# Performance work log

Hardware: AMD Instinct MI355X
Metric: run time of the kernel (lower is better)

## Reference

```python
import jax, jax.numpy as jnp
import numpy as np

L = 0.24          # lambda step size
K = 0.03          # exp(log 0.03), conductance scale used by forward
NITER = 500       # ctor Niter
DEPS = 0.1


def _g(x, k):
    # Perona-Malik conductance: 1 / (1 + |x^2| / k^2); x real so |x*x| == x*x
    return 1.0 / (1.0 + (x * x) / (k * k))


def setup_inputs() -> dict:
    key = jax.random.key(0)
    k1, k2 = jax.random.split(key)
    guide = jax.random.normal(k1, (2, 3, 512, 512), dtype=jnp.float32)
    initial = jax.random.uniform(k2, (2, 1, 512, 512), dtype=jnp.float32)
    return {"guide": guide, "initial": initial}


def reference(guide, initial):
    # shift branch (jit-safe): forward adds deps if initial.min() <= deps, subtracts at end
    shift = jnp.where(jnp.min(initial) <= DEPS, DEPS, 0.0).astype(initial.dtype)
    depth0 = initial + shift

    # conductance coefficients from guide (mean abs channel gradient), shapes:
    # cv: [B,1,H-1,W], ch: [B,1,H,W-1]
    cv = _g(jnp.mean(jnp.abs(guide[:, :, 1:, :] - guide[:, :, :-1, :]), axis=1, keepdims=True), K)
    ch = _g(jnp.mean(jnp.abs(guide[:, :, :, 1:] - guide[:, :, :, :-1]), axis=1, keepdims=True), K)

    def step(I, _):
        # both diffs computed from the same I (matches torch: dv, dh read before writes;
        # the in-place +/- updates commute, so functional adds give identical math)
        dv = I[:, :, 1:, :] - I[:, :, :-1, :]
        dh = I[:, :, :, 1:] - I[:, :, :, :-1]
        tv = L * cv * dv
        th = L * ch * dh
        I = I.at[:, :, 1:, :].add(-tv)
        I = I.at[:, :, :-1, :].add(tv)
        I = I.at[:, :, :, 1:].add(-th)
        I = I.at[:, :, :, :-1].add(th)
        return I, None

    depth, _ = jax.lax.scan(step, depth0, None, length=NITER)
    y_pred = depth - shift
    return (y_pred, cv, ch)
```

## Files before the change

kernel.cpp:

```cpp
#include <hip/hip_runtime.h>


#define HH 512
#define WW 512
#define NB 2
static constexpr float LAM   = 0.24f;
static constexpr float KCOND = 0.03f;
static constexpr float DEPS_ = 0.1f;
static constexpr int IMG      = HH * WW;
static constexpr int N_DEPTH  = NB * IMG;
static constexpr int CV_PER_B = (HH - 1) * WW;
static constexpr int CH_PER_B = HH * (WW - 1);
static constexpr int N_CV     = NB * CV_PER_B;
static constexpr int N_CH     = NB * CH_PER_B;

static constexpr int T_FUSE = 10, NSS = 50;
static constexpr int TILE_W = 64, TILE_H = 32;
static constexpr int HALO_X = 12, HALO_Y = 10;
static constexpr int RW = TILE_W + 2 * HALO_X;
static constexpr int RH = TILE_H + 2 * HALO_Y;
static constexpr int NQ_ROW = RW / 4;
static constexpr int NQUAD  = NQ_ROW * RH;
static constexpr int SSZ    = (RH + 2) * RW;

static constexpr int NT  = 512;
static constexpr int QPT = 3;
static constexpr int CVW = RW;
static constexpr int CV_SZ = (RH + 1) * CVW;
static constexpr int CHW = RW + 8;
static constexpr int CH_SZ = RH * CHW;
static constexpr int BLOB_BLK = CV_SZ + CH_SZ;

static constexpr int QPT_F = 5;

__device__ __forceinline__ unsigned fkey(float f) {
    unsigned u = __float_as_uint(f);
    return (u & 0x80000000u) ? ~u : (u | 0x80000000u);
}
__device__ __forceinline__ float kinv(unsigned k) {
    return __uint_as_float((k & 0x80000000u) ? (k & 0x7fffffffu) : ~k);
}

__global__ void init_key_kernel(unsigned* key) { *key = 0xFFFFFFFFu; }

__global__ void min_kernel(const float* __restrict__ x, unsigned* key) {
    float m = 3.4e38f;
    for (int idx = blockIdx.x * blockDim.x + threadIdx.x; idx < N_DEPTH;
         idx += gridDim.x * blockDim.x)
        m = fminf(m, x[idx]);
    for (int off = 32; off > 0; off >>= 1) m = fminf(m, __shfl_down(m, off, 64));
    __shared__ float sm[4];
    int lane = threadIdx.x & 63, wv = threadIdx.x >> 6;
    if (lane == 0) sm[wv] = m;
    __syncthreads();
    if (threadIdx.x == 0) {
        float mm = fminf(fminf(sm[0], sm[1]), fminf(sm[2], sm[3]));
        atomicMin(key, fkey(mm));
    }
}

__global__ void coeff_kernel(const float* __restrict__ g, float* __restrict__ cv,
                             float* __restrict__ chh) {
    int idx = blockIdx.x * blockDim.x + threadIdx.x;
    constexpr float kk = KCOND * KCOND;
    if (idx < N_CV) {
        int b = idx / CV_PER_B;
        int r = idx - b * CV_PER_B;
        int i = r >> 9, j = r & (WW - 1);
        const float* gb = g + b * 3 * IMG + i * WW + j;
        float s = 0.f;
#pragma unroll
        for (int c = 0; c < 3; ++c) s += fabsf(gb[c * IMG + WW] - gb[c * IMG]);
        float m = s / 3.0f;
        cv[idx] = 1.0f / (1.0f + (m * m) / kk);
    } else if (idx < N_CV + N_CH) {
        int t = idx - N_CV;
        int b = t / CH_PER_B;
        int r = t - b * CH_PER_B;
        int i = r / (WW - 1);
        int j = r - i * (WW - 1);
        const float* gb = g + b * 3 * IMG + i * WW + j;
        float s = 0.f;
#pragma unroll
        for (int c = 0; c < 3; ++c) s += fabsf(gb[c * IMG + 1] - gb[c * IMG]);
        float m = s / 3.0f;
        chh[t] = 1.0f / (1.0f + (m * m) / kk);
    }
}

__global__ __launch_bounds__(256) void prep_planes(const float* __restrict__ cv_g,
                                                   const float* __restrict__ ch_g,
                                                   float* __restrict__ blob) {
    const int blk = blockIdx.x;
    const int b   = blk >> 7, t = blk & 127;
    const int y0  = (t >> 3) * TILE_H;
    const int x0  = (t & 7) * TILE_W;
    const float* cvb = cv_g + b * CV_PER_B;
    const float* chb = ch_g + b * CH_PER_B;
    float* pv = blob + blk * BLOB_BLK;
    float* ph = pv + CV_SZ;
    for (int i = threadIdx.x; i < CV_SZ; i += 256) {
        int rr = i / CVW, x = i - rr * CVW;
        int gy = y0 - HALO_Y + rr, gx = x0 - HALO_X + x;
        bool ok = (rr >= 1) && (rr <= RH - 1) && (gy >= 1) && (gy <= HH - 1) &&
                  (gx >= 0) && (gx < WW);
        pv[i] = ok ? LAM * cvb[(gy - 1) * WW + gx] : 0.f;
    }
    for (int i = threadIdx.x; i < CH_SZ; i += 256) {
        int rr = i / CHW, xe = i - rr * CHW;
        int gy = y0 - HALO_Y + rr, gxe = x0 - HALO_X + xe;
        bool ok = (xe >= 1) && (xe <= RW - 1) && (gy >= 0) && (gy < HH) &&
                  (gxe >= 1) && (gxe < WW);
        ph[i] = ok ? LAM * chb[gy * (WW - 1) + (gxe - 1)] : 0.f;
    }
}

template <bool ADD_SHIFT, bool SUB_SHIFT>
__global__ __launch_bounds__(NT, 1) void step_fast(
    const float* __restrict__ src, float* __restrict__ dst,
    const float* __restrict__ blob, const unsigned* __restrict__ key) {
    __shared__ float sb[2][SSZ];
    const int blk = blockIdx.x;
    const int b   = blk >> 7, t = blk & 127;
    const int y0  = (t >> 3) * TILE_H;
    const int x0  = (t & 7) * TILE_W;
    const float* srcb = src + b * IMG;
    const float* pv   = blob + blk * BLOB_BLK;
    const float* ph   = pv + CV_SZ;

    float shift = 0.f;
    if (ADD_SHIFT || SUB_SHIFT) shift = (kinv(*key) <= DEPS_) ? DEPS_ : 0.f;
    const int tid = threadIdx.x;

    float v[QPT][4], cu[QPT][4], cd[QPT][4], chq[QPT][5];
    int   roff[QPT], goff[QPT];
    bool  is_int[QPT], in_img[QPT];

#pragma unroll
    for (int q = 0; q < QPT; ++q) {
        int qi   = tid + q * NT;
        bool act = qi < NQUAD;
        int qc   = act ? qi : 0;
        int r    = qc / NQ_ROW;
        int x    = (qc - r * NQ_ROW) * 4;
        roff[q]  = (r + 1) * RW + x;
        int gy = y0 - HALO_Y + r, gx = x0 - HALO_X + x;
        bool gy_in = (gy >= 0) && (gy < HH);
        in_img[q]  = act && gy_in && (gx >= 0) && (gx <= WW - 4);
        goff[q]    = in_img[q] ? (gy * WW + gx) : 0;
        is_int[q]  = act && (r >= HALO_Y) && (r < HALO_Y + TILE_H) &&
                     (x >= HALO_X) && (x < HALO_X + TILE_W);
        float4 a  = *reinterpret_cast<const float4*>(&pv[r * CVW + x]);
        float4 d  = *reinterpret_cast<const float4*>(&pv[(r + 1) * CVW + x]);
        float4 h  = *reinterpret_cast<const float4*>(&ph[r * CHW + x]);
        float  h4 = ph[r * CHW + x + 4];
        float am = act ? 1.f : 0.f;
        cu[q][0] = a.x * am; cu[q][1] = a.y * am; cu[q][2] = a.z * am; cu[q][3] = a.w * am;
        cd[q][0] = d.x * am; cd[q][1] = d.y * am; cd[q][2] = d.z * am; cd[q][3] = d.w * am;
        chq[q][0] = h.x * am; chq[q][1] = h.y * am; chq[q][2] = h.z * am;
        chq[q][3] = h.w * am; chq[q][4] = h4 * am;
        float4 tv = {0.f, 0.f, 0.f, 0.f};
        if (in_img[q]) tv = *reinterpret_cast<const float4*>(srcb + goff[q]);
        if (ADD_SHIFT && in_img[q]) {
            tv.x += shift; tv.y += shift; tv.z += shift; tv.w += shift;
        }
        v[q][0] = tv.x; v[q][1] = tv.y; v[q][2] = tv.z; v[q][3] = tv.w;
    }

    for (int i = tid; i < RW; i += NT) {
        sb[0][i] = 0.f; sb[0][(RH + 1) * RW + i] = 0.f;
        sb[1][i] = 0.f; sb[1][(RH + 1) * RW + i] = 0.f;
    }
#pragma unroll
    for (int q = 0; q < QPT; ++q)
        *reinterpret_cast<float4*>(&sb[0][roff[q]]) =
            float4{v[q][0], v[q][1], v[q][2], v[q][3]};
    __syncthreads();

    int cur = 0;
    for (int it = 0; it < T_FUSE; ++it) {
        float nv[QPT][4];
#pragma unroll
        for (int q = 0; q < QPT; ++q) {
            const float* s = sb[cur];
            float4 up = *reinterpret_cast<const float4*>(&s[roff[q] - RW]);
            float4 dn = *reinterpret_cast<const float4*>(&s[roff[q] + RW]);
            float  lf = s[roff[q] - 1];
            float  rt = s[roff[q] + 4];
            float c0 = v[q][0], c1 = v[q][1], c2 = v[q][2], c3 = v[q][3];
            nv[q][0] = c0 - cu[q][0] * (c0 - up.x) + cd[q][0] * (dn.x - c0)
                          - chq[q][0] * (c0 - lf) + chq[q][1] * (c1 - c0);
            nv[q][1] = c1 - cu[q][1] * (c1 - up.y) + cd[q][1] * (dn.y - c1)
                          - chq[q][1] * (c1 - c0) + chq[q][2] * (c2 - c1);
            nv[q][2] = c2 - cu[q][2] * (c2 - up.z) + cd[q][2] * (dn.z - c2)
                          - chq[q][2] * (c2 - c1) + chq[q][3] * (c3 - c2);
            nv[q][3] = c3 - cu[q][3] * (c3 - up.w) + cd[q][3] * (dn.w - c3)
                          - chq[q][3] * (c3 - c2) + chq[q][4] * (rt - c3);
        }
        int nxt = cur ^ 1;
#pragma unroll
        for (int q = 0; q < QPT; ++q) {
            *reinterpret_cast<float4*>(&sb[nxt][roff[q]]) =
                float4{nv[q][0], nv[q][1], nv[q][2], nv[q][3]};
            v[q][0] = nv[q][0]; v[q][1] = nv[q][1];
            v[q][2] = nv[q][2]; v[q][3] = nv[q][3];
        }
        cur = nxt;
        __syncthreads();
    }

    float* dstb = dst + b * IMG;
#pragma unroll
    for (int q = 0; q < QPT; ++q) {
        if (is_int[q]) {
            float4 o{v[q][0], v[q][1], v[q][2], v[q][3]};
            if (SUB_SHIFT) { o.x -= shift; o.y -= shift; o.z -= shift; o.w -= shift; }
            *reinterpret_cast<float4*>(dstb + goff[q]) = o;
        }
    }
}

template <bool ADD_SHIFT, bool SUB_SHIFT>
__global__ __launch_bounds__(256, 1) void step_fused(
    const float* __restrict__ src, float* __restrict__ dst,
    const float* __restrict__ cv_g, const float* __restrict__ ch_g,
    const unsigned* __restrict__ key) {
    __shared__ float sb[2][SSZ];
    const int blk = blockIdx.x;
    const int b = blk >> 7, t = blk & 127;
    const int y0 = (t >> 3) * TILE_H, x0 = (t & 7) * TILE_W;
    const float* cvb = cv_g + b * CV_PER_B;
    const float* chb = ch_g + b * CH_PER_B;
    const float* srcb = src + b * IMG;
    float* dstb = dst + b * IMG;
    float shift = 0.f;
    if (ADD_SHIFT || SUB_SHIFT) shift = (kinv(*key) <= DEPS_) ? DEPS_ : 0.f;
    const int tid = threadIdx.x;
    float v[QPT_F][4], cu[QPT_F][4], cd[QPT_F][4], chq[QPT_F][5];
    int roff[QPT_F], rr[QPT_F], xx[QPT_F];
    bool act[QPT_F];
#pragma unroll
    for (int q = 0; q < QPT_F; ++q) {
        int qi = tid + q * 256;
        act[q] = qi < NQUAD;
        int qc = act[q] ? qi : 0;
        int r = qc / NQ_ROW;
        int x = (qc - r * NQ_ROW) * 4;
        rr[q] = r; xx[q] = x;
        roff[q] = (r + 1) * RW + x;
        int gy = y0 - HALO_Y + r, gx = x0 - HALO_X + x;
        bool gy_in = (gy >= 0) && (gy < HH);
#pragma unroll
        for (int j = 0; j < 4; ++j) {
            int gxx = gx + j;
            bool gx_in = (gxx >= 0) && (gxx < WW);
            bool vin = act[q] && gy_in && gx_in;
            float val = vin ? srcb[gy * WW + gxx] : 0.f;
            if (ADD_SHIFT) val += shift;
            v[q][j] = vin ? val : 0.f;
            bool up_ok = act[q] && (r >= 1) && (gy >= 1) && (gy < HH) && gx_in;
            cu[q][j] = up_ok ? LAM * cvb[(gy - 1) * WW + gxx] : 0.f;
            bool dn_ok = act[q] && (r <= RH - 2) && (gy >= 0) && (gy < HH - 1) && gx_in;
            cd[q][j] = dn_ok ? LAM * cvb[gy * WW + gxx] : 0.f;
        }
#pragma unroll
        for (int jj = 0; jj < 5; ++jj) {
            int xe = x + jj, gxe = gx + jj;
            bool ok = act[q] && (xe >= 1) && (xe <= RW - 1) && gy_in &&
                      (gxe >= 1) && (gxe < WW);
            chq[q][jj] = ok ? LAM * chb[gy * (WW - 1) + (gxe - 1)] : 0.f;
        }
    }
    for (int i = tid; i < RW; i += 256) {
        sb[0][i] = 0.f; sb[0][(RH + 1) * RW + i] = 0.f;
        sb[1][i] = 0.f; sb[1][(RH + 1) * RW + i] = 0.f;
    }
#pragma unroll
    for (int q = 0; q < QPT_F; ++q)
        if (act[q])
            *reinterpret_cast<float4*>(&sb[0][roff[q]]) =
                float4{v[q][0], v[q][1], v[q][2], v[q][3]};
    __syncthreads();
    int cur = 0;
    for (int it = 0; it < T_FUSE; ++it) {
        float nv[QPT_F][4];
#pragma unroll
        for (int q = 0; q < QPT_F; ++q) {
            const float* s = sb[cur];
            float4 up = *reinterpret_cast<const float4*>(&s[roff[q] - RW]);
            float4 dn = *reinterpret_cast<const float4*>(&s[roff[q] + RW]);
            float lf = s[roff[q] - 1];
            float rt = s[roff[q] + 4];
            float c0 = v[q][0], c1 = v[q][1], c2 = v[q][2], c3 = v[q][3];
            nv[q][0] = c0 - cu[q][0] * (c0 - up.x) + cd[q][0] * (dn.x - c0)
                          - chq[q][0] * (c0 - lf) + chq[q][1] * (c1 - c0);
            nv[q][1] = c1 - cu[q][1] * (c1 - up.y) + cd[q][1] * (dn.y - c1)
                          - chq[q][1] * (c1 - c0) + chq[q][2] * (c2 - c1);
            nv[q][2] = c2 - cu[q][2] * (c2 - up.z) + cd[q][2] * (dn.z - c2)
                          - chq[q][2] * (c2 - c1) + chq[q][3] * (c3 - c2);
            nv[q][3] = c3 - cu[q][3] * (c3 - up.w) + cd[q][3] * (dn.w - c3)
                          - chq[q][3] * (c3 - c2) + chq[q][4] * (rt - c3);
        }
        int nxt = cur ^ 1;
#pragma unroll
        for (int q = 0; q < QPT_F; ++q) {
            if (act[q])
                *reinterpret_cast<float4*>(&sb[nxt][roff[q]]) =
                    float4{nv[q][0], nv[q][1], nv[q][2], nv[q][3]};
            v[q][0] = nv[q][0]; v[q][1] = nv[q][1];
            v[q][2] = nv[q][2]; v[q][3] = nv[q][3];
        }
        cur = nxt;
        __syncthreads();
    }
#pragma unroll
    for (int q = 0; q < QPT_F; ++q) {
        if (!act[q]) continue;
        int r = rr[q], x = xx[q];
        if (r >= HALO_Y && r < HALO_Y + TILE_H && x >= HALO_X && x < HALO_X + TILE_W) {
            int gy = y0 - HALO_Y + r, gx = x0 - HALO_X + x;
            float4 o{v[q][0], v[q][1], v[q][2], v[q][3]};
            if (SUB_SHIFT) { o.x -= shift; o.y -= shift; o.z -= shift; o.w -= shift; }
            *reinterpret_cast<float4*>(dstb + gy * WW + gx) = o;
        }
    }
}

extern "C" void kernel_launch(void* const* d_in, const int* in_sizes, int n_in,
                              void* d_out, int out_size, void* d_ws, size_t ws_size,
                              hipStream_t stream) {
    const float* guide   = (const float*)d_in[0];
    const float* initial = (const float*)d_in[1];
    float* out    = (float*)d_out;
    float* out_y  = out;
    float* out_cv = out + N_DEPTH;
    float* out_ch = out + N_DEPTH + N_CV;

    unsigned* key = (unsigned*)d_ws;
    float* wsf    = (float*)d_ws;
    float* bufA   = wsf + 64;
    float* bufB   = bufA + N_DEPTH;
    float* blob   = bufB + N_DEPTH;

    const size_t need = (size_t)(64 + 2 * N_DEPTH + 256 * BLOB_BLK) * 4;
    const bool fast = ws_size >= need;

    hipLaunchKernelGGL(init_key_kernel, dim3(1), dim3(1), 0, stream, key);
    hipLaunchKernelGGL(min_kernel, dim3(256), dim3(256), 0, stream, initial, key);

    int nco = N_CV + N_CH;
    hipLaunchKernelGGL(coeff_kernel, dim3((nco + 255) / 256), dim3(256), 0, stream,
                       guide, out_cv, out_ch);
    if (fast)
        hipLaunchKernelGGL(prep_planes, dim3(256), dim3(256), 0, stream,
                           out_cv, out_ch, blob);

    float* bufs[2] = {bufA, bufB};
    for (int k = 0; k < NSS; ++k) {
        const float* src = (k == 0) ? initial : bufs[(k + 1) & 1];
        float*       dst = (k == NSS - 1) ? out_y : bufs[k & 1];
        if (fast) {
            if (k == 0)
                hipLaunchKernelGGL((step_fast<true, false>), dim3(256), dim3(NT), 0,
                                   stream, src, dst, blob, key);
            else if (k == NSS - 1)
                hipLaunchKernelGGL((step_fast<false, true>), dim3(256), dim3(NT), 0,
                                   stream, src, dst, blob, key);
            else
                hipLaunchKernelGGL((step_fast<false, false>), dim3(256), dim3(NT), 0,
                                   stream, src, dst, blob, key);
        } else {
            if (k == 0)
                hipLaunchKernelGGL((step_fused<true, false>), dim3(256), dim3(256), 0,
                                   stream, src, dst, out_cv, out_ch, key);
            else if (k == NSS - 1)
                hipLaunchKernelGGL((step_fused<false, true>), dim3(256), dim3(256), 0,
                                   stream, src, dst, out_cv, out_ch, key);
            else
                hipLaunchKernelGGL((step_fused<false, false>), dim3(256), dim3(256), 0,
                                   stream, src, dst, out_cv, out_ch, key);
        }
    }
}
```

Measured before the change: 520.1 us.

## Register-block 4x4 pixels per thread and exchange only tile borders via LDS

Replaces the 1x4 quad-per-thread stencil with 4x4 register blocks per thread. Each thread keeps its interior neighbours in registers and publishes only its top and bottom rows and left and right columns to compact shared-memory edge buffers. Coefficients are precombined into a centre weight, so each update is a 5-term FMA sum. This cuts LDS traffic per iteration and drops block size to 320 threads, at the cost of more registers per thread and a more complex edge-buffer layout.

After: 552.3 us. 6.2% more time.

```diff
diff --git a/kernel.cpp b/kernel.cpp
--- a/kernel.cpp
+++ b/kernel.cpp
@@ -23,13 +23,21 @@
 static constexpr int NQUAD  = NQ_ROW * RH;
 static constexpr int SSZ    = (RH + 2) * RW;
 
-static constexpr int NT  = 512;
-static constexpr int QPT = 3;
 static constexpr int CVW = RW;
 static constexpr int CV_SZ = (RH + 1) * CVW;
 static constexpr int CHW = RW + 8;
 static constexpr int CH_SZ = RH * CHW;
 static constexpr int BLOB_BLK = CV_SZ + CH_SZ;
+
+static constexpr int NBAND = RH / 4;
+static constexpr int NUNIT = NBAND * NQ_ROW;
+static constexpr int NT2   = 320;
+static constexpr int RROW  = 92;
+static constexpr int RT_O  = 0;
+static constexpr int RBS_O = RT_O + (NBAND + 1) * RROW;
+static constexpr int CL_O  = RBS_O + (NBAND + 1) * RROW;
+static constexpr int CRS_O = CL_O + NBAND * 23 * 4;
+static constexpr int BUF_SZ = CRS_O + NBAND * 23 * 4;
 
 static constexpr int QPT_F = 5;
 
@@ -116,106 +124,149 @@
 }
 
 template <bool ADD_SHIFT, bool SUB_SHIFT>
-__global__ __launch_bounds__(NT, 1) void step_fast(
+__global__ __launch_bounds__(NT2, 1) void step_reg(
     const float* __restrict__ src, float* __restrict__ dst,
     const float* __restrict__ blob, const unsigned* __restrict__ key) {
-    __shared__ float sb[2][SSZ];
-    const int blk = blockIdx.x;
-    const int b   = blk >> 7, t = blk & 127;
-    const int y0  = (t >> 3) * TILE_H;
-    const int x0  = (t & 7) * TILE_W;
-    const float* srcb = src + b * IMG;
-    const float* pv   = blob + blk * BLOB_BLK;
-    const float* ph   = pv + CV_SZ;
+    __shared__ float sb[2 * BUF_SZ];
+    const int blk   = blockIdx.x;
+    const int b_img = blk >> 7, t = blk & 127;
+    const int y0 = (t >> 3) * TILE_H, x0 = (t & 7) * TILE_W;
+    const float* srcb = src + b_img * IMG;
+    const float* pv = blob + blk * BLOB_BLK;
+    const float* ph = pv + CV_SZ;
 
     float shift = 0.f;
     if (ADD_SHIFT || SUB_SHIFT) shift = (kinv(*key) <= DEPS_) ? DEPS_ : 0.f;
-    const int tid = threadIdx.x;
-
-    float v[QPT][4], cu[QPT][4], cd[QPT][4], chq[QPT][5];
-    int   roff[QPT], goff[QPT];
-    bool  is_int[QPT], in_img[QPT];
-
-#pragma unroll
-    for (int q = 0; q < QPT; ++q) {
-        int qi   = tid + q * NT;
-        bool act = qi < NQUAD;
-        int qc   = act ? qi : 0;
-        int r    = qc / NQ_ROW;
-        int x    = (qc - r * NQ_ROW) * 4;
-        roff[q]  = (r + 1) * RW + x;
-        int gy = y0 - HALO_Y + r, gx = x0 - HALO_X + x;
-        bool gy_in = (gy >= 0) && (gy < HH);
-        in_img[q]  = act && gy_in && (gx >= 0) && (gx <= WW - 4);
-        goff[q]    = in_img[q] ? (gy * WW + gx) : 0;
-        is_int[q]  = act && (r >= HALO_Y) && (r < HALO_Y + TILE_H) &&
-                     (x >= HALO_X) && (x < HALO_X + TILE_W);
-        float4 a  = *reinterpret_cast<const float4*>(&pv[r * CVW + x]);
-        float4 d  = *reinterpret_cast<const float4*>(&pv[(r + 1) * CVW + x]);
-        float4 h  = *reinterpret_cast<const float4*>(&ph[r * CHW + x]);
-        float  h4 = ph[r * CHW + x + 4];
-        float am = act ? 1.f : 0.f;
-        cu[q][0] = a.x * am; cu[q][1] = a.y * am; cu[q][2] = a.z * am; cu[q][3] = a.w * am;
-        cd[q][0] = d.x * am; cd[q][1] = d.y * am; cd[q][2] = d.z * am; cd[q][3] = d.w * am;
-        chq[q][0] = h.x * am; chq[q][1] = h.y * am; chq[q][2] = h.z * am;
-        chq[q][3] = h.w * am; chq[q][4] = h4 * am;
-        float4 tv = {0.f, 0.f, 0.f, 0.f};
-        if (in_img[q]) tv = *reinterpret_cast<const float4*>(srcb + goff[q]);
-        if (ADD_SHIFT && in_img[q]) {
-            tv.x += shift; tv.y += shift; tv.z += shift; tv.w += shift;
-        }
-        v[q][0] = tv.x; v[q][1] = tv.y; v[q][2] = tv.z; v[q][3] = tv.w;
-    }
-
-    for (int i = tid; i < RW; i += NT) {
-        sb[0][i] = 0.f; sb[0][(RH + 1) * RW + i] = 0.f;
-        sb[1][i] = 0.f; sb[1][(RH + 1) * RW + i] = 0.f;
-    }
-#pragma unroll
-    for (int q = 0; q < QPT; ++q)
-        *reinterpret_cast<float4*>(&sb[0][roff[q]]) =
-            float4{v[q][0], v[q][1], v[q][2], v[q][3]};
+
+    const int  tid = threadIdx.x;
+    const bool act = tid < NUNIT;
+    const int  u  = act ? tid : 0;
+    const int  bb = u / NQ_ROW;
+    const int  qc = u - bb * NQ_ROW;
+    const int  x  = qc * 4;
+
+    float v[4][4], vert[5][4], hz[4][5], cc[4][4];
+    int   goffr[4];
+    bool  rin[4];
+
+    const int up_o = RBS_O + bb * RROW + x;
+    const int dn_o = RT_O + (bb + 1) * RROW + x;
+    const int lf_o = CRS_O + (bb * 23 + qc) * 4;
+    const int rt_o = CL_O + (bb * 23 + qc + 1) * 4;
+    const int wt_o = RT_O + bb * RROW + x;
+    const int wb_o = RBS_O + (bb + 1) * RROW + x;
+    const int wl_o = CL_O + (bb * 23 + qc) * 4;
+    const int wr_o = CRS_O + (bb * 23 + qc + 1) * 4;
+
+    if (act) {
+#pragma unroll
+        for (int k = 0; k < 5; ++k) {
+            float4 a = *reinterpret_cast<const float4*>(&pv[(4 * bb + k) * CVW + x]);
+            vert[k][0] = a.x; vert[k][1] = a.y; vert[k][2] = a.z; vert[k][3] = a.w;
+        }
+#pragma unroll
+        for (int k = 0; k < 4; ++k) {
+            int r = 4 * bb + k;
+            float4 h = *reinterpret_cast<const float4*>(&ph[r * CHW + x]);
+            hz[k][0] = h.x; hz[k][1] = h.y; hz[k][2] = h.z; hz[k][3] = h.w;
+            hz[k][4] = ph[r * CHW + x + 4];
+        }
+#pragma unroll
+        for (int k = 0; k < 4; ++k)
+#pragma unroll
+            for (int j = 0; j < 4; ++j)
+                cc[k][j] = 1.f - (vert[k][j] + vert[k + 1][j] + hz[k][j] + hz[k][j + 1]);
+
+        int  gx    = x0 - HALO_X + x;
+        bool gx_in = (gx >= 0) && (gx <= WW - 4);
+#pragma unroll
+        for (int k = 0; k < 4; ++k) {
+            int r  = 4 * bb + k;
+            int gy = y0 - HALO_Y + r;
+            rin[k]   = gx_in && (gy >= 0) && (gy < HH);
+            goffr[k] = rin[k] ? (gy * WW + gx) : 0;
+            float4 tv = {0.f, 0.f, 0.f, 0.f};
+            if (rin[k]) tv = *reinterpret_cast<const float4*>(srcb + goffr[k]);
+            if (ADD_SHIFT && rin[k]) {
+                tv.x += shift; tv.y += shift; tv.z += shift; tv.w += shift;
+            }
+            v[k][0] = tv.x; v[k][1] = tv.y; v[k][2] = tv.z; v[k][3] = tv.w;
+        }
+    }
+
+    for (int i = tid; i < RROW; i += NT2) {
+        sb[RT_O + NBAND * RROW + i] = 0.f;
+        sb[RBS_O + i] = 0.f;
+        sb[BUF_SZ + RT_O + NBAND * RROW + i] = 0.f;
+        sb[BUF_SZ + RBS_O + i] = 0.f;
+    }
+    for (int i = tid; i < NBAND; i += NT2) {
+#pragma unroll
+        for (int j = 0; j < 4; ++j) {
+            sb[CL_O + (i * 23 + 22) * 4 + j] = 0.f;
+            sb[CRS_O + (i * 23) * 4 + j] = 0.f;
+            sb[BUF_SZ + CL_O + (i * 23 + 22) * 4 + j] = 0.f;
+            sb[BUF_SZ + CRS_O + (i * 23) * 4 + j] = 0.f;
+        }
+    }
+    if (act) {
+        *reinterpret_cast<float4*>(&sb[wt_o]) = float4{v[0][0], v[0][1], v[0][2], v[0][3]};
+        *reinterpret_cast<float4*>(&sb[wb_o]) = float4{v[3][0], v[3][1], v[3][2], v[3][3]};
+        *reinterpret_cast<float4*>(&sb[wl_o]) = float4{v[0][0], v[1][0], v[2][0], v[3][0]};
+        *reinterpret_cast<float4*>(&sb[wr_o]) = float4{v[0][3], v[1][3], v[2][3], v[3][3]};
+    }
     __syncthreads();
 
     int cur = 0;
     for (int it = 0; it < T_FUSE; ++it) {
-        float nv[QPT][4];
-#pragma unroll
-        for (int q = 0; q < QPT; ++q) {
-            const float* s = sb[cur];
-            float4 up = *reinterpret_cast<const float4*>(&s[roff[q] - RW]);
-            float4 dn = *reinterpret_cast<const float4*>(&s[roff[q] + RW]);
-            float  lf = s[roff[q] - 1];
-            float  rt = s[roff[q] + 4];
-            float c0 = v[q][0], c1 = v[q][1], c2 = v[q][2], c3 = v[q][3];
-            nv[q][0] = c0 - cu[q][0] * (c0 - up.x) + cd[q][0] * (dn.x - c0)
-                          - chq[q][0] * (c0 - lf) + chq[q][1] * (c1 - c0);
-            nv[q][1] = c1 - cu[q][1] * (c1 - up.y) + cd[q][1] * (dn.y - c1)
-                          - chq[q][1] * (c1 - c0) + chq[q][2] * (c2 - c1);
-            nv[q][2] = c2 - cu[q][2] * (c2 - up.z) + cd[q][2] * (dn.z - c2)
-                          - chq[q][2] * (c2 - c1) + chq[q][3] * (c3 - c2);
-            nv[q][3] = c3 - cu[q][3] * (c3 - up.w) + cd[q][3] * (dn.w - c3)
-                          - chq[q][3] * (c3 - c2) + chq[q][4] * (rt - c3);
-        }
         int nxt = cur ^ 1;
-#pragma unroll
-        for (int q = 0; q < QPT; ++q) {
-            *reinterpret_cast<float4*>(&sb[nxt][roff[q]]) =
-                float4{nv[q][0], nv[q][1], nv[q][2], nv[q][3]};
-            v[q][0] = nv[q][0]; v[q][1] = nv[q][1];
-            v[q][2] = nv[q][2]; v[q][3] = nv[q][3];
+        if (act) {
+            const float* bc = &sb[cur * BUF_SZ];
+            float*       bn = &sb[nxt * BUF_SZ];
+            float4 up  = *reinterpret_cast<const float4*>(&bc[up_o]);
+            float4 dn  = *reinterpret_cast<const float4*>(&bc[dn_o]);
+            float4 lf  = *reinterpret_cast<const float4*>(&bc[lf_o]);
+            float4 rt4 = *reinterpret_cast<const float4*>(&bc[rt_o]);
+            float upv[4] = {up.x, up.y, up.z, up.w};
+            float dnv[4] = {dn.x, dn.y, dn.z, dn.w};
+            float lfv[4] = {lf.x, lf.y, lf.z, lf.w};
+            float rtv[4] = {rt4.x, rt4.y, rt4.z, rt4.w};
+            float nv[4][4];
+#pragma unroll
+            for (int k = 0; k < 4; ++k) {
+#pragma unroll
+                for (int j = 0; j < 4; ++j) {
+                    float un = (k == 0) ? upv[j] : v[k - 1][j];
+                    float dd = (k == 3) ? dnv[j] : v[k + 1][j];
+                    float ll = (j == 0) ? lfv[k] : v[k][j - 1];
+                    float rr = (j == 3) ? rtv[k] : v[k][j + 1];
+                    nv[k][j] = cc[k][j] * v[k][j] + vert[k][j] * un +
+                               vert[k + 1][j] * dd + hz[k][j] * ll + hz[k][j + 1] * rr;
+                }
+            }
+            *reinterpret_cast<float4*>(&bn[wt_o]) = float4{nv[0][0], nv[0][1], nv[0][2], nv[0][3]};
+            *reinterpret_cast<float4*>(&bn[wb_o]) = float4{nv[3][0], nv[3][1], nv[3][2], nv[3][3]};
+            *reinterpret_cast<float4*>(&bn[wl_o]) = float4{nv[0][0], nv[1][0], nv[2][0], nv[3][0]};
+            *reinterpret_cast<float4*>(&bn[wr_o]) = float4{nv[0][3], nv[1][3], nv[2][3], nv[3][3]};
+#pragma unroll
+            for (int k = 0; k < 4; ++k)
+#pragma unroll
+                for (int j = 0; j < 4; ++j) v[k][j] = nv[k][j];
         }
         cur = nxt;
         __syncthreads();
     }
 
-    float* dstb = dst + b * IMG;
-#pragma unroll
-    for (int q = 0; q < QPT; ++q) {
-        if (is_int[q]) {
-            float4 o{v[q][0], v[q][1], v[q][2], v[q][3]};
-            if (SUB_SHIFT) { o.x -= shift; o.y -= shift; o.z -= shift; o.w -= shift; }
-            *reinterpret_cast<float4*>(dstb + goff[q]) = o;
+    float* dstb = dst + b_img * IMG;
+    if (act && x >= HALO_X && x < HALO_X + TILE_W) {
+#pragma unroll
+        for (int k = 0; k < 4; ++k) {
+            int r = 4 * bb + k;
+            if (r >= HALO_Y && r < HALO_Y + TILE_H) {
+                float4 o{v[k][0], v[k][1], v[k][2], v[k][3]};
+                if (SUB_SHIFT) { o.x -= shift; o.y -= shift; o.z -= shift; o.w -= shift; }
+                *reinterpret_cast<float4*>(dstb + goffr[k]) = o;
+            }
         }
     }
 }
@@ -361,13 +412,13 @@
         float*       dst = (k == NSS - 1) ? out_y : bufs[k & 1];
         if (fast) {
             if (k == 0)
-                hipLaunchKernelGGL((step_fast<true, false>), dim3(256), dim3(NT), 0,
+                hipLaunchKernelGGL((step_reg<true, false>), dim3(256), dim3(NT2), 0,
                                    stream, src, dst, blob, key);
             else if (k == NSS - 1)
-                hipLaunchKernelGGL((step_fast<false, true>), dim3(256), dim3(NT), 0,
+                hipLaunchKernelGGL((step_reg<false, true>), dim3(256), dim3(NT2), 0,
                                    stream, src, dst, blob, key);
             else
-                hipLaunchKernelGGL((step_fast<false, false>), dim3(256), dim3(NT), 0,
+                hipLaunchKernelGGL((step_reg<false, false>), dim3(256), dim3(NT2), 0,
                                    stream, src, dst, blob, key);
         } else {
             if (k == 0)
```
